# Performance work log

Hardware: AMD Instinct MI355X
Metric: run time of the kernel (lower is better)

Reference implementation:

```python
import jax, jax.numpy as jnp
import numpy as np

B, N_ATOMS, D_ATOM = 64, 256, 256
T_ANGLES = 2048
D_HID, D_OUT = 512, 256
BN_EPS = 1e-5


def setup_inputs() -> dict:
    key = jax.random.key(0)
    ks = jax.random.split(key, 8)
    z = jax.random.normal(ks[0], (B, N_ATOMS, D_ATOM), dtype=jnp.float32)
    # all entries valid (>=0) so the nonzero-selected row set is all B*T rows
    angel_atom_table = jax.random.randint(ks[1], (B, T_ANGLES, 3), 0, N_ATOMS, dtype=jnp.int64)
    W1 = jax.random.normal(ks[2], (D_ATOM, D_HID), dtype=jnp.float32) * (1.0 / np.sqrt(D_ATOM))
    b1 = jax.random.normal(ks[3], (D_HID,), dtype=jnp.float32) * 0.01
    gamma = jnp.ones((D_HID,), dtype=jnp.float32)
    beta = jnp.zeros((D_HID,), dtype=jnp.float32)
    W2 = jax.random.normal(ks[4], (D_HID, D_OUT), dtype=jnp.float32) * (1.0 / np.sqrt(D_HID))
    b2 = jax.random.normal(ks[5], (D_OUT,), dtype=jnp.float32) * 0.01
    return {"z": z, "angel_atom_table": angel_atom_table, "W1": W1, "b1": b1,
            "gamma": gamma, "beta": beta, "W2": W2, "b2": b2}


def reference(z, angel_atom_table, W1, b1, gamma, beta, W2, b2):
    Bb, Tt, _ = angel_atom_table.shape
    bi = jnp.arange(Bb)[:, None]                       # [B,1] broadcast batch index
    # gather 3 atom embeddings per angle and sum -> [B,T,d_atom]
    x = (z[bi, angel_atom_table[:, :, 0]]
         + z[bi, angel_atom_table[:, :, 1]]
         + z[bi, angel_atom_table[:, :, 2]])
    x = x.reshape(Bb * Tt, -1)                         # flattened valid rows (all valid)
    h = x @ W1 + b1                                    # Linear(d_atom, d_hid)
    mean = jnp.mean(h, axis=0)                         # BatchNorm1d (batch stats)
    var = jnp.var(h, axis=0)
    h = (h - mean) * jax.lax.rsqrt(var + BN_EPS) * gamma + beta
    h = jax.nn.relu(h)                                 # dropout inactive (eval)
    out = h @ W2 + b2                                  # Linear(d_hid, d_output)
    return out
```

## Files before the change

### kernel.cpp

```cpp
#include <hip/hip_runtime.h>

static constexpr int Bn  = 64;
static constexpr int T   = 2048;
static constexpr int NA  = 256;
static constexpr int DA  = 256;
static constexpr int DH  = 512;
static constexpr int DO  = 256;
static constexpr int M   = Bn * T;
static constexpr int NBS = M / 64;
static constexpr int NBC = M / 64;

typedef __attribute__((ext_vector_type(4))) float  f32x4;
typedef __attribute__((ext_vector_type(8))) __bf16 bf16x8;
typedef __attribute__((ext_vector_type(8))) short  short8;

__device__ __forceinline__ unsigned short f2bf(float f) {
  union { float f; unsigned u; } v; v.f = f;
  unsigned u = v.u + 0x7FFFu + ((v.u >> 16) & 1u);
  return (unsigned short)(u >> 16);
}
__device__ __forceinline__ float bf2f(unsigned short b) {
  union { unsigned u; float f; } v; v.u = ((unsigned)b) << 16;
  return v.f;
}

__global__ void prep_kernel(const float* __restrict__ W1, const float* __restrict__ W2,
                            unsigned short* __restrict__ W1T, unsigned short* __restrict__ W2T) {
  int id = blockIdx.x * 256 + threadIdx.x;
  {
    int n = id >> 8, k = id & 255;
    W1T[id] = f2bf(W1[k * DH + n]);
  }
  {
    int n = id >> 9, k = id & 511;
    W2T[id] = f2bf(W2[k * DO + n]);
  }
}

__global__ __launch_bounds__(256) void kA_zw(
    const float* __restrict__ z, const unsigned short* __restrict__ W1T,
    unsigned short* __restrict__ zW) {
  __shared__ __align__(16) unsigned short As[32][64][8];
  const int tid = threadIdx.x;
  const int xcd = blockIdx.x & 7, idx = blockIdx.x >> 3;
  const int bm = xcd * 32 + (idx >> 1), bn = idx & 1;
  const int row0 = bm * 64, n0b = bn * 256;
  const int wave = tid >> 6, lane = tid & 63, ql = lane >> 4, r16 = lane & 15;
  const int gr = tid >> 2, sub = tid & 3;
  const int sxw = (sub << 2) ^ sub;
  const int sxr = (ql << 2) ^ ql;

  const unsigned short* bp = W1T + (size_t)(n0b + wave * 64 + r16) * DA + ql * 8;

  bf16x8 bq[2][4];
#pragma unroll
  for (int p = 0; p < 2; ++p)
#pragma unroll
    for (int nf = 0; nf < 4; ++nf)
      bq[p][nf] = *(const bf16x8*)(bp + nf * 16 * DA + p * 32);

  {
    const float* zr = z + (size_t)(row0 + gr) * DA + sub * 8;
#pragma unroll
    for (int c = 0; c < 8; ++c) {
      f32x4 a0 = *(const f32x4*)(zr + c * 32);
      f32x4 a1 = *(const f32x4*)(zr + c * 32 + 4);
      bf16x8 pk;
#pragma unroll
      for (int j = 0; j < 4; ++j) { pk[j] = (__bf16)a0[j]; pk[4 + j] = (__bf16)a1[j]; }
      *(bf16x8*)&As[c * 4 + sub][gr ^ sxw][0] = pk;
    }
  }
  __syncthreads();

  f32x4 acc[4][4] = {};
#pragma unroll
  for (int s = 0; s < 8; ++s) {
    bf16x8 afr[4], bfr[4];
#pragma unroll
    for (int mf = 0; mf < 4; ++mf)
      afr[mf] = *(const bf16x8*)&As[s * 4 + ql][(mf * 16 + r16) ^ sxr][0];
#pragma unroll
    for (int nf = 0; nf < 4; ++nf) bfr[nf] = bq[s & 1][nf];
    __builtin_amdgcn_s_setprio(1);
#pragma unroll
    for (int mf = 0; mf < 4; ++mf)
#pragma unroll
      for (int nf = 0; nf < 4; ++nf)
        acc[mf][nf] = __builtin_amdgcn_mfma_f32_16x16x32_bf16(afr[mf], bfr[nf], acc[mf][nf], 0, 0, 0);
    __builtin_amdgcn_s_setprio(0);
    if (s + 2 < 8) {
#pragma unroll
      for (int nf = 0; nf < 4; ++nf)
        bq[s & 1][nf] = *(const bf16x8*)(bp + nf * 16 * DA + (s + 2) * 32);
    }
  }

  const int n0 = n0b + wave * 64;
#pragma unroll
  for (int nf = 0; nf < 4; ++nf) {
    const int col = n0 + nf * 16 + r16;
#pragma unroll
    for (int mf = 0; mf < 4; ++mf)
#pragma unroll
      for (int p = 0; p < 4; ++p)
        zW[(size_t)(row0 + mf * 16 + ql * 4 + p) * DH + col] = f2bf(acc[mf][nf][p]);
  }
}

__global__ __launch_bounds__(256) void kB_stats(
    const unsigned short* __restrict__ zW, const int* __restrict__ tbl,
    float* __restrict__ psum, float* __restrict__ psq) {
  __shared__ int idxs[64][3];
  __shared__ float red1[4][512];
  __shared__ float red2[4][512];
  const int bid = blockIdx.x;
  const int blk = (bid & 7) * (NBS >> 3) + (bid >> 3);
  const int tid = threadIdx.x;
  const int row0 = blk * 64;
  const unsigned short* zWb = zW + (size_t)(row0 >> 11) * NA * DH;

  if (tid < 192) ((int*)idxs)[tid] = tbl[(size_t)row0 * 3 + tid];
  __syncthreads();

  const int cc = tid & 63, rg = tid >> 6;
  float s1[8] = {0, 0, 0, 0, 0, 0, 0, 0};
  float s2[8] = {0, 0, 0, 0, 0, 0, 0, 0};
#pragma unroll 8
  for (int i = 0; i < 16; ++i) {
    const int r = rg * 16 + i;
    const unsigned short* p0 = zWb + (size_t)idxs[r][0] * DH + cc * 8;
    const unsigned short* p1 = zWb + (size_t)idxs[r][1] * DH + cc * 8;
    const unsigned short* p2 = zWb + (size_t)idxs[r][2] * DH + cc * 8;
    short8 v0 = *(const short8*)p0;
    short8 v1 = *(const short8*)p1;
    short8 v2 = *(const short8*)p2;
#pragma unroll
    for (int j = 0; j < 8; ++j) {
      float h = bf2f((unsigned short)v0[j]) + bf2f((unsigned short)v1[j]) + bf2f((unsigned short)v2[j]);
      s1[j] += h;
      s2[j] = fmaf(h, h, s2[j]);
    }
  }
#pragma unroll
  for (int j = 0; j < 8; ++j) { red1[rg][cc * 8 + j] = s1[j]; red2[rg][cc * 8 + j] = s2[j]; }
  __syncthreads();
  for (int c = tid; c < 512; c += 256) {
    psum[(size_t)c * NBS + blk] = red1[0][c] + red1[1][c] + red1[2][c] + red1[3][c];
    psq [(size_t)c * NBS + blk] = red2[0][c] + red2[1][c] + red2[2][c] + red2[3][c];
  }
}

__global__ void k2_stats(const float* __restrict__ psum, const float* __restrict__ psq,
                         const float* __restrict__ gamma, const float* __restrict__ beta,
                         float* __restrict__ coef) {
  const int col = blockIdx.x, lane = threadIdx.x;
  float s1 = 0.f, s2 = 0.f;
  for (int i = lane; i < NBS; i += 64) {
    s1 += psum[(size_t)col * NBS + i];
    s2 += psq [(size_t)col * NBS + i];
  }
#pragma unroll
  for (int d = 1; d < 64; d <<= 1) { s1 += __shfl_xor(s1, d); s2 += __shfl_xor(s2, d); }
  if (lane == 0) {
    const float inv = 1.0f / (float)M;
    float mean = s1 * inv;
    float var  = s2 * inv - mean * mean;
    float a = gamma[col] * rsqrtf(var + 1e-5f);
    coef[col]      = a;
    coef[DH + col] = beta[col] - mean * a;
  }
}

__global__ __launch_bounds__(256, 3) void kC_out(
    const unsigned short* __restrict__ zW, const int* __restrict__ tbl,
    const unsigned short* __restrict__ W2T, const float* __restrict__ coef,
    const float* __restrict__ b2, float* __restrict__ out) {
  __shared__ __align__(16) unsigned short As[32][64][8];
  __shared__ float aC[DH], dC[DH];
  __shared__ int idxs[64][3];

  const int bid = blockIdx.x;
  const int blk = (bid & 7) * (NBC >> 3) + (bid >> 3);
  const int tid = threadIdx.x;
  const int row0 = blk * 64;
  const unsigned short* zWb = zW + (size_t)(row0 >> 11) * NA * DH;

  if (tid < 192) ((int*)idxs)[tid] = tbl[(size_t)row0 * 3 + tid];
  aC[tid]       = coef[tid];            aC[tid + 256] = coef[tid + 256];
  dC[tid]       = coef[DH + tid];       dC[tid + 256] = coef[DH + tid + 256];
  __syncthreads();

  const int wave = tid >> 6, lane = tid & 63, ql = lane >> 4, r16 = lane & 15;
  const int gr = tid >> 2, sub = tid & 3;
  const int sxw = (sub << 2) ^ sub;
  const int sxr = (ql << 2) ^ ql;

  const unsigned short* g0p = zWb + (size_t)idxs[gr][0] * DH + sub * 8;
  const unsigned short* g1p = zWb + (size_t)idxs[gr][1] * DH + sub * 8;
  const unsigned short* g2p = zWb + (size_t)idxs[gr][2] * DH + sub * 8;

  const unsigned short* bp = W2T + (size_t)(wave * 64 + r16) * DH + ql * 8;

  bf16x8 bq[2][4];
#pragma unroll
  for (int p = 0; p < 2; ++p)
#pragma unroll
    for (int nf = 0; nf < 4; ++nf)
      bq[p][nf] = *(const bf16x8*)(bp + nf * 16 * DH + p * 32);

  f32x4 acc[4][4] = {};

#pragma unroll
  for (int h = 0; h < 2; ++h) {
    const int kh = h * 256;
    if (h) __builtin_amdgcn_s_barrier();
#pragma unroll
    for (int c = 0; c < 8; ++c) {
      short8 v0 = *(const short8*)(g0p + kh + c * 32);
      short8 v1 = *(const short8*)(g1p + kh + c * 32);
      short8 v2 = *(const short8*)(g2p + kh + c * 32);
      const int kk = kh + c * 32 + sub * 8;
      f32x4 av0 = *(const f32x4*)&aC[kk];
      f32x4 av1 = *(const f32x4*)&aC[kk + 4];
      f32x4 dv0 = *(const f32x4*)&dC[kk];
      f32x4 dv1 = *(const f32x4*)&dC[kk + 4];
      bf16x8 pk;
#pragma unroll
      for (int j = 0; j < 4; ++j) {
        float h0 = bf2f((unsigned short)v0[j]) + bf2f((unsigned short)v1[j]) + bf2f((unsigned short)v2[j]);
        float f0 = fmaf(h0, av0[j], dv0[j]);
        f0 = f0 > 0.f ? f0 : 0.f;
        pk[j] = (__bf16)f0;
        float h1 = bf2f((unsigned short)v0[4 + j]) + bf2f((unsigned short)v1[4 + j]) + bf2f((unsigned short)v2[4 + j]);
        float f1 = fmaf(h1, av1[j], dv1[j]);
        f1 = f1 > 0.f ? f1 : 0.f;
        pk[4 + j] = (__bf16)f1;
      }
      *(bf16x8*)&As[c * 4 + sub][gr ^ sxw][0] = pk;
    }
    asm volatile("s_waitcnt lgkmcnt(0)" ::: "memory");
    __builtin_amdgcn_s_barrier();
    __builtin_amdgcn_sched_barrier(0);

#pragma unroll
    for (int s = 0; s < 8; ++s) {
      const int sg = h * 8 + s;
      bf16x8 afr[4], bfr[4];
#pragma unroll
      for (int mf = 0; mf < 4; ++mf)
        afr[mf] = *(const bf16x8*)&As[s * 4 + ql][(mf * 16 + r16) ^ sxr][0];
#pragma unroll
      for (int nf = 0; nf < 4; ++nf) bfr[nf] = bq[sg & 1][nf];
      __builtin_amdgcn_s_setprio(1);
#pragma unroll
      for (int mf = 0; mf < 4; ++mf)
#pragma unroll
        for (int nf = 0; nf < 4; ++nf)
          acc[mf][nf] = __builtin_amdgcn_mfma_f32_16x16x32_bf16(afr[mf], bfr[nf], acc[mf][nf], 0, 0, 0);
      __builtin_amdgcn_s_setprio(0);
      if (sg + 2 < 16) {
#pragma unroll
        for (int nf = 0; nf < 4; ++nf)
          bq[sg & 1][nf] = *(const bf16x8*)(bp + nf * 16 * DH + (sg + 2) * 32);
      }
    }
  }

  const int n0 = wave * 64;
#pragma unroll
  for (int nf = 0; nf < 4; ++nf) {
    const int col = n0 + nf * 16 + r16;
    const float bv = b2[col];
#pragma unroll
    for (int mf = 0; mf < 4; ++mf)
#pragma unroll
      for (int p = 0; p < 4; ++p)
        out[(size_t)(row0 + mf * 16 + ql * 4 + p) * DO + col] = acc[mf][nf][p] + bv;
  }
}

extern "C" void kernel_launch(void* const* d_in, const int* in_sizes, int n_in,
                              void* d_out, int out_size, void* d_ws, size_t ws_size,
                              hipStream_t stream) {
  const float* z     = (const float*)d_in[0];
  const int*   tbl   = (const int*)d_in[1];
  const float* W1    = (const float*)d_in[2];
  const float* gamma = (const float*)d_in[4];
  const float* beta  = (const float*)d_in[5];
  const float* W2    = (const float*)d_in[6];
  const float* b2    = (const float*)d_in[7];
  float* out = (float*)d_out;

  char* ws = (char*)d_ws;
  unsigned short* W1T  = (unsigned short*)(ws);
  unsigned short* W2T  = (unsigned short*)(ws + (256 << 10));
  float*          coef = (float*)(ws + (512 << 10));
  float*          psum = (float*)(ws + (2 << 20));
  float*          psq  = (float*)(ws + (6 << 20));
  unsigned short* zW   = (unsigned short*)(ws + (16 << 20));

  prep_kernel<<<512, 256, 0, stream>>>(W1, W2, W1T, W2T);
  kA_zw<<<512, 256, 0, stream>>>(z, W1T, zW);
  kB_stats<<<NBS, 256, 0, stream>>>(zW, tbl, psum, psq);
  k2_stats<<<DH, 64, 0, stream>>>(psum, psq, gamma, beta, coef);
  kC_out<<<NBC, 256, 0, stream>>>(zW, tbl, W2T, coef, b2, out);
}
```

Baseline: 268.8 us.

## Use 512-thread blocks in GEMM kernels and halve stats block count

kA_zw and kC_out now run 8 waves per block instead of 4. Each wave computes a 64x32 output tile instead of 64x64, and the gather and convert work is split across two thread groups. The aim is more waves per CU to hide gather and global-load latency, and fewer accumulator registers per wave. kB_stats now covers 128 rows per block, which halves the partial-sum count that k2_stats must reduce. The cost is that each B fragment is reused across fewer MFMAs, giving more redundant A-fragment LDS reads per output.

```diff
diff --git a/kernel.cpp b/kernel.cpp
--- a/kernel.cpp
+++ b/kernel.cpp
@@ -7,7 +7,7 @@
 static constexpr int DH  = 512;
 static constexpr int DO  = 256;
 static constexpr int M   = Bn * T;
-static constexpr int NBS = M / 64;
+static constexpr int NBS = M / 128;
 static constexpr int NBC = M / 64;
 
 typedef __attribute__((ext_vector_type(4))) float  f32x4;
@@ -37,7 +37,7 @@
   }
 }
 
-__global__ __launch_bounds__(256) void kA_zw(
+__global__ __launch_bounds__(512, 4) void kA_zw(
     const float* __restrict__ z, const unsigned short* __restrict__ W1T,
     unsigned short* __restrict__ zW) {
   __shared__ __align__(16) unsigned short As[32][64][8];
@@ -46,59 +46,61 @@
   const int bm = xcd * 32 + (idx >> 1), bn = idx & 1;
   const int row0 = bm * 64, n0b = bn * 256;
   const int wave = tid >> 6, lane = tid & 63, ql = lane >> 4, r16 = lane & 15;
-  const int gr = tid >> 2, sub = tid & 3;
+  const int gq = tid >> 8, t8 = tid & 255;
+  const int gr = t8 >> 2, sub = t8 & 3;
   const int sxw = (sub << 2) ^ sub;
   const int sxr = (ql << 2) ^ ql;
 
-  const unsigned short* bp = W1T + (size_t)(n0b + wave * 64 + r16) * DA + ql * 8;
-
-  bf16x8 bq[2][4];
+  const unsigned short* bp = W1T + (size_t)(n0b + wave * 32 + r16) * DA + ql * 8;
+
+  bf16x8 bq[2][2];
 #pragma unroll
   for (int p = 0; p < 2; ++p)
 #pragma unroll
-    for (int nf = 0; nf < 4; ++nf)
+    for (int nf = 0; nf < 2; ++nf)
       bq[p][nf] = *(const bf16x8*)(bp + nf * 16 * DA + p * 32);
 
   {
     const float* zr = z + (size_t)(row0 + gr) * DA + sub * 8;
 #pragma unroll
-    for (int c = 0; c < 8; ++c) {
-      f32x4 a0 = *(const f32x4*)(zr + c * 32);
-      f32x4 a1 = *(const f32x4*)(zr + c * 32 + 4);
+    for (int cl = 0; cl < 4; ++cl) {
+      const int cg = gq * 4 + cl;
+      f32x4 a0 = *(const f32x4*)(zr + cg * 32);
+      f32x4 a1 = *(const f32x4*)(zr + cg * 32 + 4);
       bf16x8 pk;
 #pragma unroll
       for (int j = 0; j < 4; ++j) { pk[j] = (__bf16)a0[j]; pk[4 + j] = (__bf16)a1[j]; }
-      *(bf16x8*)&As[c * 4 + sub][gr ^ sxw][0] = pk;
+      *(bf16x8*)&As[cg * 4 + sub][gr ^ sxw][0] = pk;
     }
   }
   __syncthreads();
 
-  f32x4 acc[4][4] = {};
+  f32x4 acc[4][2] = {};
 #pragma unroll
   for (int s = 0; s < 8; ++s) {
-    bf16x8 afr[4], bfr[4];
+    bf16x8 afr[4], bfr[2];
 #pragma unroll
     for (int mf = 0; mf < 4; ++mf)
       afr[mf] = *(const bf16x8*)&As[s * 4 + ql][(mf * 16 + r16) ^ sxr][0];
 #pragma unroll
-    for (int nf = 0; nf < 4; ++nf) bfr[nf] = bq[s & 1][nf];
+    for (int nf = 0; nf < 2; ++nf) bfr[nf] = bq[s & 1][nf];
     __builtin_amdgcn_s_setprio(1);
 #pragma unroll
     for (int mf = 0; mf < 4; ++mf)
 #pragma unroll
-      for (int nf = 0; nf < 4; ++nf)
+      for (int nf = 0; nf < 2; ++nf)
         acc[mf][nf] = __builtin_amdgcn_mfma_f32_16x16x32_bf16(afr[mf], bfr[nf], acc[mf][nf], 0, 0, 0);
     __builtin_amdgcn_s_setprio(0);
     if (s + 2 < 8) {
 #pragma unroll
-      for (int nf = 0; nf < 4; ++nf)
+      for (int nf = 0; nf < 2; ++nf)
         bq[s & 1][nf] = *(const bf16x8*)(bp + nf * 16 * DA + (s + 2) * 32);
     }
   }
 
-  const int n0 = n0b + wave * 64;
-#pragma unroll
-  for (int nf = 0; nf < 4; ++nf) {
+  const int n0 = n0b + wave * 32;
+#pragma unroll
+  for (int nf = 0; nf < 2; ++nf) {
     const int col = n0 + nf * 16 + r16;
 #pragma unroll
     for (int mf = 0; mf < 4; ++mf)
@@ -111,24 +113,24 @@
 __global__ __launch_bounds__(256) void kB_stats(
     const unsigned short* __restrict__ zW, const int* __restrict__ tbl,
     float* __restrict__ psum, float* __restrict__ psq) {
-  __shared__ int idxs[64][3];
+  __shared__ int idxs[128][3];
   __shared__ float red1[4][512];
   __shared__ float red2[4][512];
   const int bid = blockIdx.x;
   const int blk = (bid & 7) * (NBS >> 3) + (bid >> 3);
   const int tid = threadIdx.x;
-  const int row0 = blk * 64;
+  const int row0 = blk * 128;
   const unsigned short* zWb = zW + (size_t)(row0 >> 11) * NA * DH;
 
-  if (tid < 192) ((int*)idxs)[tid] = tbl[(size_t)row0 * 3 + tid];
+  for (int i = tid; i < 384; i += 256) ((int*)idxs)[i] = tbl[(size_t)row0 * 3 + i];
   __syncthreads();
 
   const int cc = tid & 63, rg = tid >> 6;
   float s1[8] = {0, 0, 0, 0, 0, 0, 0, 0};
   float s2[8] = {0, 0, 0, 0, 0, 0, 0, 0};
 #pragma unroll 8
-  for (int i = 0; i < 16; ++i) {
-    const int r = rg * 16 + i;
+  for (int i = 0; i < 32; ++i) {
+    const int r = rg * 32 + i;
     const unsigned short* p0 = zWb + (size_t)idxs[r][0] * DH + cc * 8;
     const unsigned short* p1 = zWb + (size_t)idxs[r][1] * DH + cc * 8;
     const unsigned short* p2 = zWb + (size_t)idxs[r][2] * DH + cc * 8;
@@ -172,7 +174,7 @@
   }
 }
 
-__global__ __launch_bounds__(256, 3) void kC_out(
+__global__ __launch_bounds__(512, 4) void kC_out(
     const unsigned short* __restrict__ zW, const int* __restrict__ tbl,
     const unsigned short* __restrict__ W2T, const float* __restrict__ coef,
     const float* __restrict__ b2, float* __restrict__ out) {
@@ -187,12 +189,13 @@
   const unsigned short* zWb = zW + (size_t)(row0 >> 11) * NA * DH;
 
   if (tid < 192) ((int*)idxs)[tid] = tbl[(size_t)row0 * 3 + tid];
-  aC[tid]       = coef[tid];            aC[tid + 256] = coef[tid + 256];
-  dC[tid]       = coef[DH + tid];       dC[tid + 256] = coef[DH + tid + 256];
+  aC[tid] = coef[tid];
+  dC[tid] = coef[DH + tid];
   __syncthreads();
 
   const int wave = tid >> 6, lane = tid & 63, ql = lane >> 4, r16 = lane & 15;
-  const int gr = tid >> 2, sub = tid & 3;
+  const int gq = tid >> 8, t8 = tid & 255;
+  const int gr = t8 >> 2, sub = t8 & 3;
   const int sxw = (sub << 2) ^ sub;
   const int sxr = (ql << 2) ^ ql;
 
@@ -200,27 +203,27 @@
   const unsigned short* g1p = zWb + (size_t)idxs[gr][1] * DH + sub * 8;
   const unsigned short* g2p = zWb + (size_t)idxs[gr][2] * DH + sub * 8;
 
-  const unsigned short* bp = W2T + (size_t)(wave * 64 + r16) * DH + ql * 8;
-
-  bf16x8 bq[2][4];
+  const unsigned short* bp = W2T + (size_t)(wave * 32 + r16) * DH + ql * 8;
+
+  bf16x8 bq[2][2];
 #pragma unroll
   for (int p = 0; p < 2; ++p)
 #pragma unroll
-    for (int nf = 0; nf < 4; ++nf)
+    for (int nf = 0; nf < 2; ++nf)
       bq[p][nf] = *(const bf16x8*)(bp + nf * 16 * DH + p * 32);
 
-  f32x4 acc[4][4] = {};
+  f32x4 acc[4][2] = {};
 
 #pragma unroll
   for (int h = 0; h < 2; ++h) {
-    const int kh = h * 256;
     if (h) __builtin_amdgcn_s_barrier();
 #pragma unroll
-    for (int c = 0; c < 8; ++c) {
-      short8 v0 = *(const short8*)(g0p + kh + c * 32);
-      short8 v1 = *(const short8*)(g1p + kh + c * 32);
-      short8 v2 = *(const short8*)(g2p + kh + c * 32);
-      const int kk = kh + c * 32 + sub * 8;
+    for (int cl = 0; cl < 4; ++cl) {
+      const int coff = h * 256 + (gq * 4 + cl) * 32;
+      short8 v0 = *(const short8*)(g0p + coff);
+      short8 v1 = *(const short8*)(g1p + coff);
+      short8 v2 = *(const short8*)(g2p + coff);
+      const int kk = coff + sub * 8;
       f32x4 av0 = *(const f32x4*)&aC[kk];
       f32x4 av1 = *(const f32x4*)&aC[kk + 4];
       f32x4 dv0 = *(const f32x4*)&dC[kk];
@@ -237,7 +240,7 @@
         f1 = f1 > 0.f ? f1 : 0.f;
         pk[4 + j] = (__bf16)f1;
       }
-      *(bf16x8*)&As[c * 4 + sub][gr ^ sxw][0] = pk;
+      *(bf16x8*)&As[(gq * 4 + cl) * 4 + sub][gr ^ sxw][0] = pk;
     }
     asm volatile("s_waitcnt lgkmcnt(0)" ::: "memory");
     __builtin_amdgcn_s_barrier();
@@ -246,30 +249,30 @@
 #pragma unroll
     for (int s = 0; s < 8; ++s) {
       const int sg = h * 8 + s;
-      bf16x8 afr[4], bfr[4];
+      bf16x8 afr[4], bfr[2];
 #pragma unroll
       for (int mf = 0; mf < 4; ++mf)
         afr[mf] = *(const bf16x8*)&As[s * 4 + ql][(mf * 16 + r16) ^ sxr][0];
 #pragma unroll
-      for (int nf = 0; nf < 4; ++nf) bfr[nf] = bq[sg & 1][nf];
+      for (int nf = 0; nf < 2; ++nf) bfr[nf] = bq[sg & 1][nf];
       __builtin_amdgcn_s_setprio(1);
 #pragma unroll
       for (int mf = 0; mf < 4; ++mf)
 #pragma unroll
-        for (int nf = 0; nf < 4; ++nf)
+        for (int nf = 0; nf < 2; ++nf)
           acc[mf][nf] = __builtin_amdgcn_mfma_f32_16x16x32_bf16(afr[mf], bfr[nf], acc[mf][nf], 0, 0, 0);
       __builtin_amdgcn_s_setprio(0);
       if (sg + 2 < 16) {
 #pragma unroll
-        for (int nf = 0; nf < 4; ++nf)
+        for (int nf = 0; nf < 2; ++nf)
           bq[sg & 1][nf] = *(const bf16x8*)(bp + nf * 16 * DH + (sg + 2) * 32);
       }
     }
   }
 
-  const int n0 = wave * 64;
-#pragma unroll
-  for (int nf = 0; nf < 4; ++nf) {
+  const int n0 = wave * 32;
+#pragma unroll
+  for (int nf = 0; nf < 2; ++nf) {
     const int col = n0 + nf * 16 + r16;
     const float bv = b2[col];
 #pragma unroll
@@ -297,12 +300,12 @@
   unsigned short* W2T  = (unsigned short*)(ws + (256 << 10));
   float*          coef = (float*)(ws + (512 << 10));
   float*          psum = (float*)(ws + (2 << 20));
-  float*          psq  = (float*)(ws + (6 << 20));
+  float*          psq  = (float*)(ws + (4 << 20));
   unsigned short* zW   = (unsigned short*)(ws + (16 << 20));
 
   prep_kernel<<<512, 256, 0, stream>>>(W1, W2, W1T, W2T);
-  kA_zw<<<512, 256, 0, stream>>>(z, W1T, zW);
+  kA_zw<<<512, 512, 0, stream>>>(z, W1T, zW);
   kB_stats<<<NBS, 256, 0, stream>>>(zW, tbl, psum, psq);
   k2_stats<<<DH, 64, 0, stream>>>(psum, psq, gamma, beta, coef);
-  kC_out<<<NBC, 256, 0, stream>>>(zW, tbl, W2T, coef, b2, out);
-}
+  kC_out<<<NBC, 512, 0, stream>>>(zW, tbl, W2T, coef, b2, out);
+}
```

After: 268.5 us. No clear change (-0.1%).
